# Optimization experiments

Hardware: AMD Instinct MI355X
Metric: run time of the kernel (lower is better)

Reference implementation:

```python
import jax, jax.numpy as jnp
import numpy as np

EPS = 1e-5
SEQ = 64

def ln(x, g, b):
    m = jnp.mean(x, axis=-1, keepdims=True)
    v = jnp.var(x, axis=-1, keepdims=True)
    return (x - m) / jnp.sqrt(v + EPS) * g + b

def gelu(x):
    return jax.nn.gelu(x, approximate=False)  # torch nn.GELU default = exact erf

def setup_inputs() -> dict:
    key = jax.random.key(0)
    ks = jax.random.split(key, 24)
    B, D = 512, 128
    DSGU = 4 * D          # 512
    DATTN = DSGU // 2     # 256
    DEXP = 4 * D          # 512 (tiny-attn expanded dim)
    TF = SEQ * D          # 8192
    H = int(1.1 * TF)     # 9011
    w = lambda k, s: jax.random.normal(k, s, dtype=jnp.float32) * 0.02
    return {
        "x": jax.random.normal(ks[0], (B, SEQ, D), dtype=jnp.float32),
        # TinyAttentionBlock
        "qkv_ln_g": jnp.ones((D,), jnp.float32), "qkv_ln_b": jnp.zeros((D,), jnp.float32),
        "qkv_w": w(ks[1], (D, 3 * DEXP)), "qkv_b": jnp.zeros((3 * DEXP,), jnp.float32),
        "attn_proj_w": w(ks[2], (DEXP, DATTN)), "attn_proj_b": jnp.zeros((DATTN,), jnp.float32),
        "attn_ln_g": jnp.ones((DATTN,), jnp.float32), "attn_ln_b": jnp.zeros((DATTN,), jnp.float32),
        "rel_bias": w(ks[3], (2 * SEQ - 1,)),
        "scale": jnp.asarray(1.0 / np.sqrt(D), jnp.float32),
        # SGU proj_in / proj_spatial / proj_out
        "pin_ln_g": jnp.ones((D,), jnp.float32), "pin_ln_b": jnp.zeros((D,), jnp.float32),
        "pin_w": w(ks[4], (D, DSGU)), "pin_b": jnp.zeros((DSGU,), jnp.float32),
        "sp_ln_g": jnp.ones((SEQ,), jnp.float32), "sp_ln_b": jnp.zeros((SEQ,), jnp.float32),
        "sp_w": w(ks[5], (SEQ, SEQ)), "sp_b": jnp.ones((SEQ,), jnp.float32),  # bias init 1.0 per source
        "pout_ln_g": jnp.ones((DATTN,), jnp.float32), "pout_ln_b": jnp.zeros((DATTN,), jnp.float32),
        "pout_w": w(ks[6], (DATTN, D)), "pout_b": jnp.zeros((D,), jnp.float32),
        # ResidualBlock MLP
        "mlp_ln_g": jnp.ones((TF,), jnp.float32), "mlp_ln_b": jnp.zeros((TF,), jnp.float32),
        "mlp_w1": w(ks[7], (TF, H)), "mlp_b1": jnp.zeros((H,), jnp.float32),
        "mlp_w2": w(ks[8], (H, TF)), "mlp_b2": jnp.zeros((TF,), jnp.float32),
    }

def reference(x, qkv_ln_g, qkv_ln_b, qkv_w, qkv_b, attn_proj_w, attn_proj_b,
              attn_ln_g, attn_ln_b, rel_bias, scale,
              pin_ln_g, pin_ln_b, pin_w, pin_b, sp_ln_g, sp_ln_b, sp_w, sp_b,
              pout_ln_g, pout_ln_b, pout_w, pout_b,
              mlp_ln_g, mlp_ln_b, mlp_w1, mlp_b1, mlp_w2, mlp_b2):
    B = x.shape[0]
    # --- TinyAttentionBlock ---
    h = ln(x, qkv_ln_g, qkv_ln_b) @ qkv_w + qkv_b          # [B,64,3*512]
    q, k, v = jnp.split(h, 3, axis=-1)                      # each [B,64,512]
    idx = jnp.arange(SEQ)
    rel = idx[None, :] - idx[:, None] + (SEQ - 1)           # [64,64] in [0,126]
    bias = rel_bias[rel]                                    # [64,64]
    attn = jnp.einsum('bnd,bmd->bnm', q, k) + bias
    attn = jax.nn.softmax(attn, axis=-1) * scale            # post-softmax scale (as in source)
    av = jnp.einsum('bnm,bmd->bnd', attn, v)                # [B,64,512]
    a = ln(av @ attn_proj_w + attn_proj_b, attn_ln_g, attn_ln_b)  # [B,64,256]
    # --- SpatialGatingUnit ---
    h2 = gelu(ln(x, pin_ln_g, pin_ln_b) @ pin_w + pin_b)    # [B,64,512]
    u, vv = jnp.split(h2, 2, axis=-1)                        # [B,64,256] each
    vt = jnp.swapaxes(vv, 1, 2)                              # [B,256,64]
    vt = gelu(ln(vt, sp_ln_g, sp_ln_b) @ sp_w + sp_b)        # spatial proj over seq dim
    vv = jnp.swapaxes(vt, 1, 2)                              # [B,64,256]
    out = u * (vv + a)
    out = ln(out, pout_ln_g, pout_ln_b) @ pout_w + pout_b    # [B,64,128]
    x = x + out
    # --- ResidualBlock MLP on flattened board ---
    xf = x.reshape(B, -1)                                    # [B,8192]
    h3 = gelu(ln(xf, mlp_ln_g, mlp_ln_b) @ mlp_w1 + mlp_b1)  # [B,9011]
    xf = xf + (h3 @ mlp_w2 + mlp_b2)
    return xf.reshape(B, SEQ, -1)
```

## Files before the change

kernel.cpp:

```cpp
#include <hip/hip_runtime.h>
#include <hip/hip_bf16.h>
#include <math.h>

typedef float f32x4 __attribute__((ext_vector_type(4)));
typedef float f32x2 __attribute__((ext_vector_type(2)));
typedef short s16x8 __attribute__((ext_vector_type(8)));
typedef short s16x4 __attribute__((ext_vector_type(4)));
typedef int   i32x4 __attribute__((ext_vector_type(4)));

__device__ __forceinline__ short f2bf(float f) {
  __hip_bfloat16 h = __float2bfloat16(f);
  return __builtin_bit_cast(short, h);
}
__device__ __forceinline__ float bf2f(short s) {
  __hip_bfloat16 h = __builtin_bit_cast(__hip_bfloat16, s);
  return __bfloat162float(h);
}
__device__ __forceinline__ float gelu_f(float x) {
  return 0.5f * x * (1.f + erff(x * 0.70710678118654752440f));
}
__device__ __forceinline__ float waveSum(float v) {
  #pragma unroll
  for (int d = 32; d; d >>= 1) v += __shfl_xor(v, d);
  return v;
}
__device__ __forceinline__ void softBarrier() {
  asm volatile("s_waitcnt lgkmcnt(0)" ::: "memory");
  __builtin_amdgcn_s_barrier();
  asm volatile("" ::: "memory");
}

__global__ __launch_bounds__(256) void fused_attn_k(
    const float* __restrict__ x,
    const float* __restrict__ qln_g, const float* __restrict__ qln_b,
    const float* __restrict__ pln_g, const float* __restrict__ pln_b,
    const float* __restrict__ qkv_w, const float* __restrict__ qkv_b,
    const float* __restrict__ attn_pw, const float* __restrict__ attn_pb,
    const float* __restrict__ aln_g, const float* __restrict__ aln_b,
    const float* __restrict__ relb, const float* __restrict__ scale_p,
    short* __restrict__ lnp, float* __restrict__ ab)
{
  __shared__ __align__(16) char arena[153088];
  short (*lnq)[136]  = reinterpret_cast<short(*)[136]>(arena + 0);
  short (*plds)[72]  = reinterpret_cast<short(*)[72]>(arena + 17408);
  short (*vlds)[72]  = reinterpret_cast<short(*)[72]>(arena + 26624);
  short (*avl)[136]  = reinterpret_cast<short(*)[136]>(arena + 26624);
  short (*qlds)[136] = reinterpret_cast<short(*)[136]>(arena + 45056);
  short (*klds)[136] = reinterpret_cast<short(*)[136]>(arena + 62464);
  short (*pwT)[128]  = reinterpret_cast<short(*)[128]>(arena + 45056);
  short (*wT)[128]   = reinterpret_cast<short(*)[128]>(arena + 110592);
  float* rb    = reinterpret_cast<float*>(arena + 143360);
  float* s_apb = reinterpret_cast<float*>(arena + 143872);
  float* s_ag  = reinterpret_cast<float*>(arena + 144896);
  float* s_ab2 = reinterpret_cast<float*>(arena + 145920);
  float* sqb   = reinterpret_cast<float*>(arena + 146944);

  const int t = threadIdx.x, lane = t & 63, w = t >> 6;
  const int ln15 = lane & 15, hi = lane >> 4;
  const int b = blockIdx.x;

  if (t < 127) rb[t] = relb[t];
  s_apb[t] = attn_pb[t]; s_ag[t] = aln_g[t]; s_ab2[t] = aln_b[t];
  #pragma unroll
  for (int i = 0; i < 6; ++i) sqb[i*256 + t] = qkv_b[i*256 + t];

  {
    int c = lane * 2;
    float qg0 = qln_g[c], qg1 = qln_g[c+1], qb0 = qln_b[c], qb1 = qln_b[c+1];
    float pg0 = pln_g[c], pg1 = pln_g[c+1], pb0 = pln_b[c], pb1 = pln_b[c+1];
    for (int i = 0; i < 16; ++i) {
      int r = w * 16 + i;
      f32x2 v = *reinterpret_cast<const f32x2*>(&x[((size_t)b*64 + r)*128 + c]);
      float s = v[0] + v[1], sq = v[0]*v[0] + v[1]*v[1];
      s = waveSum(s); sq = waveSum(sq);
      float m = s * (1.f/128.f);
      float rstd = rsqrtf(sq*(1.f/128.f) - m*m + 1e-5f);
      float a0 = (v[0]-m)*rstd, a1 = (v[1]-m)*rstd;
      unsigned q0 = (unsigned short)f2bf(a0*qg0 + qb0);
      unsigned q1 = (unsigned short)f2bf(a1*qg1 + qb1);
      *reinterpret_cast<unsigned*>(&lnq[r][c]) = q0 | (q1 << 16);
      unsigned p0 = (unsigned short)f2bf(a0*pg0 + pb0);
      unsigned p1 = (unsigned short)f2bf(a1*pg1 + pb1);
      ((unsigned*)lnp)[((size_t)b*64 + r)*64 + lane] = p0 | (p1 << 16);
    }
  }
  __syncthreads();

  auto stageW = [&](int coff) {
    const int c = t & 127, h = t >> 7;
    #pragma unroll
    for (int j = 0; j < 8; ++j) {
      int o = h * 8 + j;
      s16x8 v;
      #pragma unroll
      for (int m = 0; m < 8; ++m)
        v[m] = f2bf(qkv_w[(size_t)(o*8 + m) * 1536 + coff + c]);
      int os = (o & 8) | ((o & 7) ^ (c & 7));
      *reinterpret_cast<s16x8*>(&wT[c][os * 8]) = v;
    }
  };
  auto stagePW = [&](int cc) {
    const int c = t;
    #pragma unroll
    for (int o = 0; o < 16; ++o) {
      s16x8 v;
      #pragma unroll
      for (int m = 0; m < 8; ++m)
        v[m] = f2bf(attn_pw[(size_t)(cc*128 + o*8 + m) * 256 + c]);
      int os = (o & 8) | ((o & 7) ^ (c & 7));
      *reinterpret_cast<s16x8*>(&pwT[c][os * 8]) = v;
    }
  };
  auto gemm8 = [&](f32x4 (&acc)[8]) {
    #pragma unroll
    for (int kk = 0; kk < 4; ++kk) {
      s16x8 af = *reinterpret_cast<const s16x8*>(&lnq[w*16 + ln15][kk*32 + hi*8]);
      const int o = kk*4 + hi;
      #pragma unroll
      for (int fn = 0; fn < 8; ++fn) {
        int col = fn*16 + ln15;
        int os = (o & 8) | ((o & 7) ^ (col & 7));
        s16x8 bf = *reinterpret_cast<const s16x8*>(&wT[col][os * 8]);
        acc[fn] = __builtin_amdgcn_mfma_f32_16x16x32_bf16(af, bf, acc[fn], 0, 0, 0);
      }
    }
  };

  f32x4 sacc[4] = {};
  for (int kc = 0; kc < 4; ++kc) {
    __syncthreads();
    stageW(kc * 128);
    __syncthreads();
    {
      f32x4 qa[8] = {};
      gemm8(qa);
      #pragma unroll
      for (int fn = 0; fn < 8; ++fn) {
        float bias = sqb[kc*128 + fn*16 + ln15];
        #pragma unroll
        for (int j = 0; j < 4; ++j)
          qlds[w*16 + hi*4 + j][fn*16 + ln15] = f2bf(qa[fn][j] + bias);
      }
    }
    __syncthreads();
    stageW(512 + kc * 128);
    __syncthreads();
    {
      f32x4 ka[8] = {};
      gemm8(ka);
      #pragma unroll
      for (int fn = 0; fn < 8; ++fn) {
        float bias = sqb[512 + kc*128 + fn*16 + ln15];
        #pragma unroll
        for (int j = 0; j < 4; ++j)
          klds[w*16 + hi*4 + j][fn*16 + ln15] = f2bf(ka[fn][j] + bias);
      }
    }
    __syncthreads();
    #pragma unroll
    for (int kk = 0; kk < 4; ++kk) {
      s16x8 aq = *reinterpret_cast<const s16x8*>(&qlds[16*w + ln15][kk*32 + hi*8]);
      #pragma unroll
      for (int fn = 0; fn < 4; ++fn) {
        s16x8 bk = *reinterpret_cast<const s16x8*>(&klds[fn*16 + ln15][kk*32 + hi*8]);
        sacc[fn] = __builtin_amdgcn_mfma_f32_16x16x32_bf16(aq, bk, sacc[fn], 0, 0, 0);
      }
    }
  }

  {
    float scale = scale_p[0];
    #pragma unroll
    for (int j = 0; j < 4; ++j) {
      int row = 16*w + hi*4 + j;
      float pv[4];
      float mx = -1e30f;
      #pragma unroll
      for (int fn = 0; fn < 4; ++fn) {
        int col = fn*16 + ln15;
        pv[fn] = sacc[fn][j] + rb[col - row + 63];
        mx = fmaxf(mx, pv[fn]);
      }
      #pragma unroll
      for (int d = 1; d < 16; d <<= 1) mx = fmaxf(mx, __shfl_xor(mx, d));
      float sum = 0.f;
      #pragma unroll
      for (int fn = 0; fn < 4; ++fn) { pv[fn] = __expf(pv[fn] - mx); sum += pv[fn]; }
      #pragma unroll
      for (int d = 1; d < 16; d <<= 1) sum += __shfl_xor(sum, d);
      float inv = scale / sum;
      #pragma unroll
      for (int fn = 0; fn < 4; ++fn) plds[row][fn*16 + ln15] = f2bf(pv[fn] * inv);
    }
  }

  f32x4 pracc[16] = {};
  for (int cc = 0; cc < 4; ++cc) {
    __syncthreads();
    stageW(1024 + cc * 128);
    stagePW(cc);
    __syncthreads();
    {
      f32x4 va[8] = {};
      gemm8(va);
      #pragma unroll
      for (int fn = 0; fn < 8; ++fn) {
        float bias = sqb[1024 + cc*128 + fn*16 + ln15];
        s16x4 vv;
        #pragma unroll
        for (int j = 0; j < 4; ++j) vv[j] = f2bf(va[fn][j] + bias);
        *reinterpret_cast<s16x4*>(&vlds[fn*16 + ln15][w*16 + hi*4]) = vv;
      }
    }
    __syncthreads();
    f32x4 pacc[8] = {};
    #pragma unroll
    for (int kk = 0; kk < 2; ++kk) {
      s16x8 ap = *reinterpret_cast<const s16x8*>(&plds[16*w + ln15][kk*32 + hi*8]);
      #pragma unroll
      for (int fn = 0; fn < 8; ++fn) {
        s16x8 bv = *reinterpret_cast<const s16x8*>(&vlds[fn*16 + ln15][kk*32 + hi*8]);
        pacc[fn] = __builtin_amdgcn_mfma_f32_16x16x32_bf16(ap, bv, pacc[fn], 0, 0, 0);
      }
    }
    __syncthreads();
    #pragma unroll
    for (int fn = 0; fn < 8; ++fn)
      #pragma unroll
      for (int j = 0; j < 4; ++j)
        avl[w*16 + hi*4 + j][fn*16 + ln15] = f2bf(pacc[fn][j]);
    __syncthreads();
    #pragma unroll
    for (int kk = 0; kk < 4; ++kk) {
      s16x8 aa = *reinterpret_cast<const s16x8*>(&avl[16*w + ln15][kk*32 + hi*8]);
      const int o = kk*4 + hi;
      #pragma unroll
      for (int fn = 0; fn < 16; ++fn) {
        int col = fn*16 + ln15;
        int os = (o & 8) | ((o & 7) ^ (col & 7));
        s16x8 pb = *reinterpret_cast<const s16x8*>(&pwT[col][os * 8]);
        pracc[fn] = __builtin_amdgcn_mfma_f32_16x16x32_bf16(aa, pb, pracc[fn], 0, 0, 0);
      }
    }
  }

  #pragma unroll
  for (int j = 0; j < 4; ++j) {
    int row = 16*w + hi*4 + j;
    float vv[16];
    float s = 0.f, sq = 0.f;
    #pragma unroll
    for (int fn = 0; fn < 16; ++fn) {
      vv[fn] = pracc[fn][j] + s_apb[fn*16 + ln15];
      s += vv[fn]; sq += vv[fn]*vv[fn];
    }
    #pragma unroll
    for (int d = 1; d < 16; d <<= 1) { s += __shfl_xor(s, d); sq += __shfl_xor(sq, d); }
    float m = s * (1.f/256.f);
    float rstd = rsqrtf(sq*(1.f/256.f) - m*m + 1e-5f);
    #pragma unroll
    for (int fn = 0; fn < 16; ++fn) {
      int col = fn*16 + ln15;
      ab[((size_t)b*64 + row)*256 + col] = (vv[fn]-m)*rstd*s_ag[col] + s_ab2[col];
    }
  }
}

template<int BM, int BN, int WM, int WN, int EPI>
__global__ __launch_bounds__(256) void gemm_k(
    const short* __restrict__ A, const float* __restrict__ Bw,
    const float* __restrict__ bias, const float* __restrict__ res,
    void* __restrict__ O0, void* __restrict__ O1,
    int M, int N, int K, int Nreal, int Kreal)
{
  constexpr int BK = 64;
  __shared__ __align__(16) short As[BM][BK + 8];
  __shared__ __align__(16) short Bs[BN][BK + 8];
  const int t = threadIdx.x;
  const int lane = t & 63;
  const int w = t >> 6;
  const int wm = w / WN, wn = w % WN;
  const int ln15 = lane & 15, hi = lane >> 4;
  const int m0 = blockIdx.y * BM;
  const int n0 = blockIdx.x * BN;

  f32x4 acc[4][4] = {};

  for (int k0 = 0; k0 < K; k0 += BK) {
    #pragma unroll
    for (int i = 0; i < (BM*BK)/(256*8); ++i) {
      int e = (i*256 + t) * 8;
      int r = e / BK, c = e % BK;
      *reinterpret_cast<i32x4*>(&As[r][c]) =
          *reinterpret_cast<const i32x4*>(&A[(size_t)(m0 + r) * K + k0 + c]);
    }
    #pragma unroll
    for (int i = 0; i < (BK*BN)/256; ++i) {
      int idx = i*256 + t;
      int n = idx % BN, k = idx / BN;
      int gk = k0 + k, gn = n0 + n;
      float v = (gk < Kreal && gn < Nreal) ? Bw[(size_t)gk * Nreal + gn] : 0.f;
      Bs[n][k] = f2bf(v);
    }
    __syncthreads();
    #pragma unroll
    for (int kk = 0; kk < BK; kk += 32) {
      s16x8 af[4], bfr[4];
      #pragma unroll
      for (int fm = 0; fm < 4; ++fm)
        af[fm] = *reinterpret_cast<const s16x8*>(&As[wm*64 + fm*16 + ln15][kk + hi*8]);
      #pragma unroll
      for (int fn = 0; fn < 4; ++fn)
        bfr[fn] = *reinterpret_cast<const s16x8*>(&Bs[wn*64 + fn*16 + ln15][kk + hi*8]);
      #pragma unroll
      for (int fm = 0; fm < 4; ++fm)
        #pragma unroll
        for (int fn = 0; fn < 4; ++fn)
          acc[fm][fn] = __builtin_amdgcn_mfma_f32_16x16x32_bf16(
              af[fm], bfr[fn], acc[fm][fn], 0, 0, 0);
    }
    __syncthreads();
  }

  #pragma unroll
  for (int fm = 0; fm < 4; ++fm) {
    #pragma unroll
    for (int fn = 0; fn < 4; ++fn) {
      #pragma unroll
      for (int j = 0; j < 4; ++j) {
        int row = m0 + wm*64 + fm*16 + hi*4 + j;
        int col = n0 + wn*64 + fn*16 + ln15;
        float v = acc[fm][fn][j];
        if constexpr (EPI == 2) {
          v = gelu_f(v + bias[col]);
          if (col < 256) ((float*)O0)[(size_t)row * 256 + col] = v;
          else ((short*)O1)[(size_t)row * 256 + (col - 256)] = f2bf(v);
        } else {
          v += bias[col] + res[(size_t)row * N + col];
          ((float*)O0)[(size_t)row * N + col] = v;
        }
      }
    }
  }
}

__global__ __launch_bounds__(256) void ln8192_k(
    const float* __restrict__ x1,
    const float* __restrict__ g, const float* __restrict__ bb,
    short* __restrict__ lnxp)
{
  __shared__ float red[8];
  int t = threadIdx.x, w = t >> 6, lane = t & 63;
  int b = blockIdx.x;
  const f32x4* xr = reinterpret_cast<const f32x4*>(x1 + (size_t)b * 8192);
  f32x4 vals[8];
  float s = 0.f, sq = 0.f;
  #pragma unroll
  for (int i = 0; i < 8; ++i) {
    f32x4 v = xr[t + i*256];
    vals[i] = v;
    s  += v[0]+v[1]+v[2]+v[3];
    sq += v[0]*v[0]+v[1]*v[1]+v[2]*v[2]+v[3]*v[3];
  }
  s = waveSum(s); sq = waveSum(sq);
  if (lane == 0) { red[w] = s; red[4+w] = sq; }
  __syncthreads();
  s  = red[0]+red[1]+red[2]+red[3];
  sq = red[4]+red[5]+red[6]+red[7];
  float m = s * (1.f/8192.f);
  float rstd = rsqrtf(sq * (1.f/8192.f) - m*m + 1e-5f);
  #pragma unroll
  for (int i = 0; i < 8; ++i) {
    int idx = (t + i*256) * 4;
    f32x4 g4 = reinterpret_cast<const f32x4*>(g)[t + i*256];
    f32x4 b4 = reinterpret_cast<const f32x4*>(bb)[t + i*256];
    s16x4 o;
    #pragma unroll
    for (int k = 0; k < 4; ++k) o[k] = f2bf((vals[i][k]-m)*rstd*g4[k] + b4[k]);
    size_t paddr = ((size_t)(idx >> 6) * 512 + b) * 64 + (idx & 63);
    *reinterpret_cast<s16x4*>(&lnxp[paddr]) = o;
  }
}

__global__ __launch_bounds__(512, 2) void gemm_splitk9(
    const short* __restrict__ Ap, const float* __restrict__ Bw,
    float* __restrict__ part,
    int N, int K, int Kreal, int ldb, int kchunk, int ntiles)
{
  __shared__ __align__(16) short Bs[2][128 * 64];
  const int t = threadIdx.x, lane = t & 63, w = t >> 6;
  const int ln15 = lane & 15, hi = lane >> 4;
  const int nt = blockIdx.x % ntiles, z = blockIdx.x / ntiles;
  const int n0 = nt * 128;
  const int kbeg = z * kchunk;
  const int kend = (kbeg + kchunk < K) ? (kbeg + kchunk) : K;
  const int nsteps = (kend - kbeg) >> 6;

  const int bn = t & 127;
  const int bg0 = (t >> 7) * 2;
  const bool bok = (n0 + bn) < ldb;
  const int bsw = bn & 7;

  float br[16];
  auto loadB = [&](int k0) {
    const float* bp = Bw + (size_t)(k0 + bg0 * 8) * ldb + n0 + bn;
    #pragma unroll
    for (int m = 0; m < 16; ++m) {
      int gk = k0 + bg0 * 8 + m;
      br[m] = (bok && gk < Kreal) ? bp[(size_t)m * ldb] : 0.f;
    }
  };
  auto writeB = [&](int buf) {
    s16x8 v0, v1;
    #pragma unroll
    for (int m = 0; m < 8; ++m) { v0[m] = f2bf(br[m]); v1[m] = f2bf(br[8 + m]); }
    short* dst = &Bs[buf][bn * 64];
    *reinterpret_cast<s16x8*>(dst + ((bg0    ) ^ bsw) * 8) = v0;
    *reinterpret_cast<s16x8*>(dst + ((bg0 + 1) ^ bsw) * 8) = v1;
  };

  f32x4 acc[4][8] = {};

  loadB(kbeg);
  writeB(0);
  if (nsteps > 1) loadB(kbeg + 64);
  softBarrier();

  for (int s = 0; s < nsteps; ++s) {
    const int k0 = kbeg + s * 64;
    const short* atile = Ap + (size_t)(k0 >> 6) * 512 * 64;
    s16x8 af[8];
    #pragma unroll
    for (int kk = 0; kk < 2; ++kk)
      #pragma unroll
      for (int fm = 0; fm < 4; ++fm) {
        int row = w * 64 + fm * 16 + ln15;
        af[kk * 4 + fm] = *reinterpret_cast<const s16x8*>(
            &atile[row * 64 + (kk * 4 + hi) * 8]);
      }
    if (s + 1 < nsteps) writeB((s + 1) & 1);
    if (s + 2 < nsteps) loadB(kbeg + (s + 2) * 64);

    const short* bsrc = &Bs[s & 1][0];
    #pragma unroll
    for (int kk = 0; kk < 2; ++kk) {
      const int g = kk * 4 + hi;
      #pragma unroll
      for (int fn = 0; fn < 8; ++fn) {
        int row = fn * 16 + ln15;
        s16x8 bv = *reinterpret_cast<const s16x8*>(
            &bsrc[row * 64 + ((g ^ (row & 7)) * 8)]);
        #pragma unroll
        for (int fm = 0; fm < 4; ++fm)
          acc[fm][fn] = __builtin_amdgcn_mfma_f32_16x16x32_bf16(
              af[kk * 4 + fm], bv, acc[fm][fn], 0, 0, 0);
      }
    }
    softBarrier();
  }

  #pragma unroll
  for (int fm = 0; fm < 4; ++fm)
    #pragma unroll
    for (int fn = 0; fn < 8; ++fn)
      #pragma unroll
      for (int j = 0; j < 4; ++j) {
        int row = w * 64 + fm * 16 + hi * 4 + j;
        int col = n0 + fn * 16 + ln15;
        part[((size_t)z * 512 + row) * N + col] = acc[fm][fn][j];
      }
}

__global__ __launch_bounds__(256) void reduce_mlp1_k(
    const float* __restrict__ part, const float* __restrict__ bias,
    short* __restrict__ h3p, int N, int Nreal, int M, int ks)
{
  int col4 = (blockIdx.x * 256 + threadIdx.x) * 4;
  int row = blockIdx.y;
  if (col4 >= N) return;
  size_t base = (size_t)row * N + col4;
  size_t stride = (size_t)M * N;
  f32x4 s = *reinterpret_cast<const f32x4*>(part + base);
  for (int k = 1; k < ks; ++k)
    s += *reinterpret_cast<const f32x4*>(part + base + (size_t)k * stride);
  s16x4 o;
  #pragma unroll
  for (int j = 0; j < 4; ++j) {
    int c = col4 + j;
    float v = 0.f;
    if (c < Nreal) v = gelu_f(s[j] + bias[c]);
    o[j] = f2bf(v);
  }
  size_t paddr = ((size_t)(col4 >> 6) * 512 + row) * 64 + (col4 & 63);
  *reinterpret_cast<s16x4*>(&h3p[paddr]) = o;
}

__global__ __launch_bounds__(256) void reduce_mlp2_k(
    const float* __restrict__ part, const float* __restrict__ bias,
    const float* __restrict__ x1, float* __restrict__ out, int N, int M, int ks)
{
  int col4 = (blockIdx.x * 256 + threadIdx.x) * 4;
  int row = blockIdx.y;
  size_t base = (size_t)row * N + col4;
  size_t stride = (size_t)M * N;
  f32x4 s = *reinterpret_cast<const f32x4*>(part + base);
  for (int k = 1; k < ks; ++k)
    s += *reinterpret_cast<const f32x4*>(part + base + (size_t)k * stride);
  f32x4 b4 = *reinterpret_cast<const f32x4*>(bias + col4);
  f32x4 r4 = *reinterpret_cast<const f32x4*>(x1 + base);
  #pragma unroll
  for (int j = 0; j < 4; ++j) s[j] += b4[j] + r4[j];
  *reinterpret_cast<f32x4*>(out + base) = s;
}

__global__ __launch_bounds__(256) void gate_k(
    const float* __restrict__ u, const short* __restrict__ vbf,
    const float* __restrict__ a,
    const float* __restrict__ spg_g, const float* __restrict__ spg_b,
    const float* __restrict__ spw, const float* __restrict__ spb,
    const float* __restrict__ pog, const float* __restrict__ pob,
    short* __restrict__ outn)
{
  __shared__ __align__(16) short nvb[256][72];
  __shared__ __align__(16) short spwT[64][72];
  __shared__ float s_spg[64], s_spbl[64], s_spb[64];
  __shared__ float s_pog[256], s_pob[256];
  int t = threadIdx.x, lane = t & 63, w = t >> 6;
  int ln15 = lane & 15, hi = lane >> 4;
  int b = blockIdx.x;

  if (t < 64) { s_spg[t] = spg_g[t]; s_spbl[t] = spg_b[t]; s_spb[t] = spb[t]; }
  s_pog[t] = pog[t]; s_pob[t] = pob[t];
  #pragma unroll
  for (int i = 0; i < 16; ++i) {
    int idx = i*256 + t;
    int sr = idx >> 6, tc = idx & 63;
    spwT[tc][sr] = f2bf(spw[idx]);
  }

  float vvv[64];
  {
    int c = t;
    float s = 0.f, sq = 0.f;
    #pragma unroll
    for (int si = 0; si < 64; ++si) {
      float f = bf2f(vbf[(size_t)(b*64 + si) * 256 + c]);
      vvv[si] = f; s += f; sq += f*f;
    }
    float m = s * (1.f/64.f);
    float rstd = rsqrtf(sq * (1.f/64.f) - m*m + 1e-5f);
    __syncthreads();
    #pragma unroll
    for (int si = 0; si < 64; ++si)
      nvb[c][si] = f2bf((vvv[si]-m)*rstd*s_spg[si] + s_spbl[si]);
  }
  __syncthreads();

  f32x4 yacc[4][4] = {};
  #pragma unroll
  for (int kk = 0; kk < 64; kk += 32) {
    s16x8 af[4], bfr[4];
    #pragma unroll
    for (int fm = 0; fm < 4; ++fm)
      af[fm] = *reinterpret_cast<const s16x8*>(&nvb[64*w + fm*16 + ln15][kk + hi*8]);
    #pragma unroll
    for (int fn = 0; fn < 4; ++fn)
      bfr[fn] = *reinterpret_cast<const s16x8*>(&spwT[fn*16 + ln15][kk + hi*8]);
    #pragma unroll
    for (int fm = 0; fm < 4; ++fm)
      #pragma unroll
      for (int fn = 0; fn < 4; ++fn)
        yacc[fm][fn] = __builtin_amdgcn_mfma_f32_16x16x32_bf16(
            af[fm], bfr[fn], yacc[fm][fn], 0, 0, 0);
  }
  __syncthreads();

  short (*outl)[264] = reinterpret_cast<short(*)[264]>(&nvb[0][0]);
  #pragma unroll
  for (int fm = 0; fm < 4; ++fm) {
    #pragma unroll
    for (int fn = 0; fn < 4; ++fn) {
      int crow = 64*w + fm*16 + hi*4;
      int tcol = fn*16 + ln15;
      f32x4 u4 = *reinterpret_cast<const f32x4*>(&u[(size_t)(b*64 + tcol)*256 + crow]);
      f32x4 a4 = *reinterpret_cast<const f32x4*>(&a[(size_t)(b*64 + tcol)*256 + crow]);
      #pragma unroll
      for (int j = 0; j < 4; ++j) {
        float g = gelu_f(yacc[fm][fn][j] + s_spb[tcol]);
        float o = u4[j] * (g + a4[j]);
        outl[tcol][crow + j] = f2bf(o);
      }
    }
  }
  __syncthreads();

  #pragma unroll
  for (int ri = 0; ri < 16; ++ri) {
    int trow = w*16 + ri;
    int c = lane * 4;
    s16x4 raw = *reinterpret_cast<const s16x4*>(&outl[trow][c]);
    float f0 = bf2f(raw[0]), f1 = bf2f(raw[1]), f2 = bf2f(raw[2]), f3 = bf2f(raw[3]);
    float s  = f0+f1+f2+f3;
    float sq = f0*f0+f1*f1+f2*f2+f3*f3;
    s = waveSum(s); sq = waveSum(sq);
    float m = s * (1.f/256.f);
    float rstd = rsqrtf(sq * (1.f/256.f) - m*m + 1e-5f);
    s16x4 o;
    o[0] = f2bf((f0-m)*rstd*s_pog[c+0] + s_pob[c+0]);
    o[1] = f2bf((f1-m)*rstd*s_pog[c+1] + s_pob[c+1]);
    o[2] = f2bf((f2-m)*rstd*s_pog[c+2] + s_pob[c+2]);
    o[3] = f2bf((f3-m)*rstd*s_pog[c+3] + s_pob[c+3]);
    *reinterpret_cast<s16x4*>(&outn[(size_t)(b*64 + trow)*256 + c]) = o;
  }
}

extern "C" void kernel_launch(void* const* d_in, const int* in_sizes, int n_in,
                              void* d_out, int out_size, void* d_ws, size_t ws_size,
                              hipStream_t stream)
{
  const float* x          = (const float*)d_in[0];
  const float* qkv_ln_g   = (const float*)d_in[1];
  const float* qkv_ln_b   = (const float*)d_in[2];
  const float* qkv_w      = (const float*)d_in[3];
  const float* qkv_b      = (const float*)d_in[4];
  const float* attn_pw    = (const float*)d_in[5];
  const float* attn_pb    = (const float*)d_in[6];
  const float* attn_ln_g  = (const float*)d_in[7];
  const float* attn_ln_b  = (const float*)d_in[8];
  const float* rel_bias   = (const float*)d_in[9];
  const float* scale      = (const float*)d_in[10];
  const float* pin_ln_g   = (const float*)d_in[11];
  const float* pin_ln_b   = (const float*)d_in[12];
  const float* pin_w      = (const float*)d_in[13];
  const float* pin_b      = (const float*)d_in[14];
  const float* sp_ln_g    = (const float*)d_in[15];
  const float* sp_ln_b    = (const float*)d_in[16];
  const float* sp_w       = (const float*)d_in[17];
  const float* sp_b       = (const float*)d_in[18];
  const float* pout_ln_g  = (const float*)d_in[19];
  const float* pout_ln_b  = (const float*)d_in[20];
  const float* pout_w     = (const float*)d_in[21];
  const float* pout_b     = (const float*)d_in[22];
  const float* mlp_ln_g   = (const float*)d_in[23];
  const float* mlp_ln_b   = (const float*)d_in[24];
  const float* mlp_w1     = (const float*)d_in[25];
  const float* mlp_b1     = (const float*)d_in[26];
  const float* mlp_w2     = (const float*)d_in[27];
  const float* mlp_b2     = (const float*)d_in[28];

  char* ws = (char*)d_ws;
  short* lnp   = (short*)(ws + 0);
  float* x1b   = (float*)(ws + 0);
  float* ab    = (float*)(ws + 16777216);
  float* ub    = (float*)(ws + 50331648);
  short* vbfb  = (short*)(ws + 83886080);
  short* outnb = (short*)(ws + 100663296);
  short* lnxp  = (short*)(ws + 150994944);
  short* h3p   = (short*)(ws + 159383552);
  float* partb = (float*)(ws + 16777216);

  fused_attn_k<<<512, 256, 0, stream>>>(
      x, qkv_ln_g, qkv_ln_b, pin_ln_g, pin_ln_b, qkv_w, qkv_b,
      attn_pw, attn_pb, attn_ln_g, attn_ln_b, rel_bias, scale, lnp, ab);
  gemm_k<128,128,2,2,2><<<dim3(4,256), 256, 0, stream>>>(
      lnp, pin_w, pin_b, nullptr, ub, vbfb, 32768, 512, 128, 512, 128);
  gate_k<<<512, 256, 0, stream>>>(ub, vbfb, ab, sp_ln_g, sp_ln_b, sp_w, sp_b,
                                  pout_ln_g, pout_ln_b, outnb);
  gemm_k<128,128,2,2,3><<<dim3(1,256), 256, 0, stream>>>(
      outnb, pout_w, pout_b, x, x1b, nullptr, 32768, 128, 256, 128, 256);
  ln8192_k<<<512, 256, 0, stream>>>(x1b, mlp_ln_g, mlp_ln_b, lnxp);

  gemm_splitk9<<<213, 512, 0, stream>>>(
      lnxp, mlp_w1, partb, 9088, 8192, 8192,
      9011, 2752, 71);
  reduce_mlp1_k<<<dim3(9, 512), 256, 0, stream>>>(partb, mlp_b1, h3p, 9088, 9011, 512, 3);

  gemm_splitk9<<<256, 512, 0, stream>>>(
      h3p, mlp_w2, partb, 8192, 9088, 9011,
      8192, 2304, 64);
  reduce_mlp2_k<<<dim3(8, 512), 256, 0, stream>>>(partb, mlp_b2, x1b, (float*)d_out, 8192, 512, 4);
}
```

Baseline: 718.6 us.

## Pre-transpose attention weights to bf16 once and read them from global in fused attention

Adds a small prep kernel that converts the qkv and attention-projection weights to transposed bf16 once per call. The fused attention kernel then reads MFMA B-operands directly from global/L2 instead of staging and converting the weights into LDS in every block. This shrinks LDS from about 150KB to about 73KB so two blocks can share a CU, and it reworks the QK loop into 64-wide chunks. The cost is one extra launch and operand loads that are uncoalesced global reads rather than LDS reads.

```diff
diff --git a/kernel.cpp b/kernel.cpp
--- a/kernel.cpp
+++ b/kernel.cpp
@@ -30,37 +30,58 @@
   asm volatile("" ::: "memory");
 }
 
-__global__ __launch_bounds__(256) void fused_attn_k(
+__global__ __launch_bounds__(256) void prep_w_k(
+    const float* __restrict__ qkv_w, const float* __restrict__ attn_pw,
+    short* __restrict__ wTg, short* __restrict__ pwTg)
+{
+  int idx = blockIdx.x * 256 + threadIdx.x;
+  if (idx < 24576) {
+    int r = idx >> 4;
+    int k0 = (idx & 15) * 8;
+    s16x8 v;
+    #pragma unroll
+    for (int m = 0; m < 8; ++m) v[m] = f2bf(qkv_w[(size_t)(k0 + m) * 1536 + r]);
+    *reinterpret_cast<s16x8*>(&wTg[r * 128 + k0]) = v;
+  } else if (idx < 24576 + 16384) {
+    int e = idx - 24576;
+    int r = e >> 6;
+    int k0 = (e & 63) * 8;
+    s16x8 v;
+    #pragma unroll
+    for (int m = 0; m < 8; ++m) v[m] = f2bf(attn_pw[(size_t)(k0 + m) * 256 + r]);
+    *reinterpret_cast<s16x8*>(&pwTg[r * 512 + k0]) = v;
+  }
+}
+
+__global__ __launch_bounds__(256, 2) void fused_attn_k(
     const float* __restrict__ x,
     const float* __restrict__ qln_g, const float* __restrict__ qln_b,
     const float* __restrict__ pln_g, const float* __restrict__ pln_b,
-    const float* __restrict__ qkv_w, const float* __restrict__ qkv_b,
-    const float* __restrict__ attn_pw, const float* __restrict__ attn_pb,
+    const short* __restrict__ wTg, const float* __restrict__ qkv_b,
+    const short* __restrict__ pwTg, const float* __restrict__ attn_pb,
     const float* __restrict__ aln_g, const float* __restrict__ aln_b,
     const float* __restrict__ relb, const float* __restrict__ scale_p,
     short* __restrict__ lnp, float* __restrict__ ab)
 {
-  __shared__ __align__(16) char arena[153088];
-  short (*lnq)[136]  = reinterpret_cast<short(*)[136]>(arena + 0);
-  short (*plds)[72]  = reinterpret_cast<short(*)[72]>(arena + 17408);
-  short (*vlds)[72]  = reinterpret_cast<short(*)[72]>(arena + 26624);
-  short (*avl)[136]  = reinterpret_cast<short(*)[136]>(arena + 26624);
-  short (*qlds)[136] = reinterpret_cast<short(*)[136]>(arena + 45056);
-  short (*klds)[136] = reinterpret_cast<short(*)[136]>(arena + 62464);
-  short (*pwT)[128]  = reinterpret_cast<short(*)[128]>(arena + 45056);
-  short (*wT)[128]   = reinterpret_cast<short(*)[128]>(arena + 110592);
-  float* rb    = reinterpret_cast<float*>(arena + 143360);
-  float* s_apb = reinterpret_cast<float*>(arena + 143872);
-  float* s_ag  = reinterpret_cast<float*>(arena + 144896);
-  float* s_ab2 = reinterpret_cast<float*>(arena + 145920);
-  float* sqb   = reinterpret_cast<float*>(arena + 146944);
+  __shared__ __align__(16) char arena[73216];
+  short (*lnq)[136] = reinterpret_cast<short(*)[136]>(arena + 0);
+  short (*vlds)[72] = reinterpret_cast<short(*)[72]>(arena + 17408);
+  short (*avl)[136] = reinterpret_cast<short(*)[136]>(arena + 17408);
+  short (*q64)[72]  = reinterpret_cast<short(*)[72]>(arena + 35840);
+  short (*k64)[72]  = reinterpret_cast<short(*)[72]>(arena + 45056);
+  short (*p64)[72]  = reinterpret_cast<short(*)[72]>(arena + 54272);
+  float* sqb  = reinterpret_cast<float*>(arena + 63488);
+  float* rb   = reinterpret_cast<float*>(arena + 69632);
+  float* sapb = reinterpret_cast<float*>(arena + 70144);
+  float* sag  = reinterpret_cast<float*>(arena + 71168);
+  float* sab2 = reinterpret_cast<float*>(arena + 72192);
 
   const int t = threadIdx.x, lane = t & 63, w = t >> 6;
   const int ln15 = lane & 15, hi = lane >> 4;
   const int b = blockIdx.x;
 
   if (t < 127) rb[t] = relb[t];
-  s_apb[t] = attn_pb[t]; s_ag[t] = aln_g[t]; s_ab2[t] = aln_b[t];
+  sapb[t] = attn_pb[t]; sag[t] = aln_g[t]; sab2[t] = aln_b[t];
   #pragma unroll
   for (int i = 0; i < 6; ++i) sqb[i*256 + t] = qkv_b[i*256 + t];
 
@@ -76,9 +97,9 @@
       float m = s * (1.f/128.f);
       float rstd = rsqrtf(sq*(1.f/128.f) - m*m + 1e-5f);
       float a0 = (v[0]-m)*rstd, a1 = (v[1]-m)*rstd;
-      unsigned q0 = (unsigned short)f2bf(a0*qg0 + qb0);
-      unsigned q1 = (unsigned short)f2bf(a1*qg1 + qb1);
-      *reinterpret_cast<unsigned*>(&lnq[r][c]) = q0 | (q1 << 16);
+      unsigned u0 = (unsigned short)f2bf(a0*qg0 + qb0);
+      unsigned u1 = (unsigned short)f2bf(a1*qg1 + qb1);
+      *reinterpret_cast<unsigned*>(&lnq[r][c]) = u0 | (u1 << 16);
       unsigned p0 = (unsigned short)f2bf(a0*pg0 + pb0);
       unsigned p1 = (unsigned short)f2bf(a1*pg1 + pb1);
       ((unsigned*)lnp)[((size_t)b*64 + r)*64 + lane] = p0 | (p1 << 16);
@@ -86,83 +107,59 @@
   }
   __syncthreads();
 
-  auto stageW = [&](int coff) {
-    const int c = t & 127, h = t >> 7;
-    #pragma unroll
-    for (int j = 0; j < 8; ++j) {
-      int o = h * 8 + j;
-      s16x8 v;
-      #pragma unroll
-      for (int m = 0; m < 8; ++m)
-        v[m] = f2bf(qkv_w[(size_t)(o*8 + m) * 1536 + coff + c]);
-      int os = (o & 8) | ((o & 7) ^ (c & 7));
-      *reinterpret_cast<s16x8*>(&wT[c][os * 8]) = v;
-    }
-  };
-  auto stagePW = [&](int cc) {
-    const int c = t;
-    #pragma unroll
-    for (int o = 0; o < 16; ++o) {
-      s16x8 v;
-      #pragma unroll
-      for (int m = 0; m < 8; ++m)
-        v[m] = f2bf(attn_pw[(size_t)(cc*128 + o*8 + m) * 256 + c]);
-      int os = (o & 8) | ((o & 7) ^ (c & 7));
-      *reinterpret_cast<s16x8*>(&pwT[c][os * 8]) = v;
-    }
-  };
-  auto gemm8 = [&](f32x4 (&acc)[8]) {
+  auto gemm4g = [&](int coff, f32x4 (&acc)[4]) {
     #pragma unroll
     for (int kk = 0; kk < 4; ++kk) {
       s16x8 af = *reinterpret_cast<const s16x8*>(&lnq[w*16 + ln15][kk*32 + hi*8]);
-      const int o = kk*4 + hi;
+      #pragma unroll
+      for (int fn = 0; fn < 4; ++fn) {
+        int col = coff + fn*16 + ln15;
+        s16x8 bf = *reinterpret_cast<const s16x8*>(&wTg[(size_t)col*128 + kk*32 + hi*8]);
+        acc[fn] = __builtin_amdgcn_mfma_f32_16x16x32_bf16(af, bf, acc[fn], 0, 0, 0);
+      }
+    }
+  };
+  auto gemm8g = [&](int coff, f32x4 (&acc)[8]) {
+    #pragma unroll
+    for (int kk = 0; kk < 4; ++kk) {
+      s16x8 af = *reinterpret_cast<const s16x8*>(&lnq[w*16 + ln15][kk*32 + hi*8]);
       #pragma unroll
       for (int fn = 0; fn < 8; ++fn) {
-        int col = fn*16 + ln15;
-        int os = (o & 8) | ((o & 7) ^ (col & 7));
-        s16x8 bf = *reinterpret_cast<const s16x8*>(&wT[col][os * 8]);
+        int col = coff + fn*16 + ln15;
+        s16x8 bf = *reinterpret_cast<const s16x8*>(&wTg[(size_t)col*128 + kk*32 + hi*8]);
         acc[fn] = __builtin_amdgcn_mfma_f32_16x16x32_bf16(af, bf, acc[fn], 0, 0, 0);
       }
     }
   };
 
   f32x4 sacc[4] = {};
-  for (int kc = 0; kc < 4; ++kc) {
-    __syncthreads();
-    stageW(kc * 128);
-    __syncthreads();
-    {
-      f32x4 qa[8] = {};
-      gemm8(qa);
-      #pragma unroll
-      for (int fn = 0; fn < 8; ++fn) {
-        float bias = sqb[kc*128 + fn*16 + ln15];
-        #pragma unroll
-        for (int j = 0; j < 4; ++j)
-          qlds[w*16 + hi*4 + j][fn*16 + ln15] = f2bf(qa[fn][j] + bias);
-      }
-    }
-    __syncthreads();
-    stageW(512 + kc * 128);
-    __syncthreads();
-    {
-      f32x4 ka[8] = {};
-      gemm8(ka);
-      #pragma unroll
-      for (int fn = 0; fn < 8; ++fn) {
-        float bias = sqb[512 + kc*128 + fn*16 + ln15];
-        #pragma unroll
-        for (int j = 0; j < 4; ++j)
-          klds[w*16 + hi*4 + j][fn*16 + ln15] = f2bf(ka[fn][j] + bias);
-      }
-    }
-    __syncthreads();
-    #pragma unroll
-    for (int kk = 0; kk < 4; ++kk) {
-      s16x8 aq = *reinterpret_cast<const s16x8*>(&qlds[16*w + ln15][kk*32 + hi*8]);
+  for (int kc = 0; kc < 8; ++kc) {
+    __syncthreads();
+    f32x4 qa[4] = {};
+    gemm4g(kc * 64, qa);
+    #pragma unroll
+    for (int fn = 0; fn < 4; ++fn) {
+      float bias = sqb[kc*64 + fn*16 + ln15];
+      #pragma unroll
+      for (int j = 0; j < 4; ++j)
+        q64[w*16 + hi*4 + j][fn*16 + ln15] = f2bf(qa[fn][j] + bias);
+    }
+    f32x4 ka[4] = {};
+    gemm4g(512 + kc * 64, ka);
+    #pragma unroll
+    for (int fn = 0; fn < 4; ++fn) {
+      float bias = sqb[512 + kc*64 + fn*16 + ln15];
+      #pragma unroll
+      for (int j = 0; j < 4; ++j)
+        k64[w*16 + hi*4 + j][fn*16 + ln15] = f2bf(ka[fn][j] + bias);
+    }
+    __syncthreads();
+    #pragma unroll
+    for (int kk = 0; kk < 2; ++kk) {
+      s16x8 aq = *reinterpret_cast<const s16x8*>(&q64[16*w + ln15][kk*32 + hi*8]);
       #pragma unroll
       for (int fn = 0; fn < 4; ++fn) {
-        s16x8 bk = *reinterpret_cast<const s16x8*>(&klds[fn*16 + ln15][kk*32 + hi*8]);
+        s16x8 bk = *reinterpret_cast<const s16x8*>(&k64[fn*16 + ln15][kk*32 + hi*8]);
         sacc[fn] = __builtin_amdgcn_mfma_f32_16x16x32_bf16(aq, bk, sacc[fn], 0, 0, 0);
       }
     }
@@ -190,33 +187,28 @@
       for (int d = 1; d < 16; d <<= 1) sum += __shfl_xor(sum, d);
       float inv = scale / sum;
       #pragma unroll
-      for (int fn = 0; fn < 4; ++fn) plds[row][fn*16 + ln15] = f2bf(pv[fn] * inv);
+      for (int fn = 0; fn < 4; ++fn) p64[row][fn*16 + ln15] = f2bf(pv[fn] * inv);
     }
   }
 
   f32x4 pracc[16] = {};
   for (int cc = 0; cc < 4; ++cc) {
     __syncthreads();
-    stageW(1024 + cc * 128);
-    stagePW(cc);
-    __syncthreads();
-    {
-      f32x4 va[8] = {};
-      gemm8(va);
-      #pragma unroll
-      for (int fn = 0; fn < 8; ++fn) {
-        float bias = sqb[1024 + cc*128 + fn*16 + ln15];
-        s16x4 vv;
-        #pragma unroll
-        for (int j = 0; j < 4; ++j) vv[j] = f2bf(va[fn][j] + bias);
-        *reinterpret_cast<s16x4*>(&vlds[fn*16 + ln15][w*16 + hi*4]) = vv;
-      }
+    f32x4 va[8] = {};
+    gemm8g(1024 + cc * 128, va);
+    #pragma unroll
+    for (int fn = 0; fn < 8; ++fn) {
+      float bias = sqb[1024 + cc*128 + fn*16 + ln15];
+      s16x4 vv;
+      #pragma unroll
+      for (int j = 0; j < 4; ++j) vv[j] = f2bf(va[fn][j] + bias);
+      *reinterpret_cast<s16x4*>(&vlds[fn*16 + ln15][w*16 + hi*4]) = vv;
     }
     __syncthreads();
     f32x4 pacc[8] = {};
     #pragma unroll
     for (int kk = 0; kk < 2; ++kk) {
-      s16x8 ap = *reinterpret_cast<const s16x8*>(&plds[16*w + ln15][kk*32 + hi*8]);
+      s16x8 ap = *reinterpret_cast<const s16x8*>(&p64[16*w + ln15][kk*32 + hi*8]);
       #pragma unroll
       for (int fn = 0; fn < 8; ++fn) {
         s16x8 bv = *reinterpret_cast<const s16x8*>(&vlds[fn*16 + ln15][kk*32 + hi*8]);
@@ -233,12 +225,10 @@
     #pragma unroll
     for (int kk = 0; kk < 4; ++kk) {
       s16x8 aa = *reinterpret_cast<const s16x8*>(&avl[16*w + ln15][kk*32 + hi*8]);
-      const int o = kk*4 + hi;
       #pragma unroll
       for (int fn = 0; fn < 16; ++fn) {
-        int col = fn*16 + ln15;
-        int os = (o & 8) | ((o & 7) ^ (col & 7));
-        s16x8 pb = *reinterpret_cast<const s16x8*>(&pwT[col][os * 8]);
+        s16x8 pb = *reinterpret_cast<const s16x8*>(
+            &pwTg[(size_t)(fn*16 + ln15)*512 + cc*128 + kk*32 + hi*8]);
         pracc[fn] = __builtin_amdgcn_mfma_f32_16x16x32_bf16(aa, pb, pracc[fn], 0, 0, 0);
       }
     }
@@ -251,7 +241,7 @@
     float s = 0.f, sq = 0.f;
     #pragma unroll
     for (int fn = 0; fn < 16; ++fn) {
-      vv[fn] = pracc[fn][j] + s_apb[fn*16 + ln15];
+      vv[fn] = pracc[fn][j] + sapb[fn*16 + ln15];
       s += vv[fn]; sq += vv[fn]*vv[fn];
     }
     #pragma unroll
@@ -261,7 +251,7 @@
     #pragma unroll
     for (int fn = 0; fn < 16; ++fn) {
       int col = fn*16 + ln15;
-      ab[((size_t)b*64 + row)*256 + col] = (vv[fn]-m)*rstd*s_ag[col] + s_ab2[col];
+      ab[((size_t)b*64 + row)*256 + col] = (vv[fn]-m)*rstd*sag[col] + sab2[col];
     }
   }
 }
@@ -653,15 +643,18 @@
   float* x1b   = (float*)(ws + 0);
   float* ab    = (float*)(ws + 16777216);
   float* ub    = (float*)(ws + 50331648);
+  short* wTg   = (short*)(ws + 83886080);
+  short* pwTg  = (short*)(ws + 84279296);
   short* vbfb  = (short*)(ws + 83886080);
   short* outnb = (short*)(ws + 100663296);
   short* lnxp  = (short*)(ws + 150994944);
   short* h3p   = (short*)(ws + 159383552);
   float* partb = (float*)(ws + 16777216);
 
+  prep_w_k<<<160, 256, 0, stream>>>(qkv_w, attn_pw, wTg, pwTg);
   fused_attn_k<<<512, 256, 0, stream>>>(
-      x, qkv_ln_g, qkv_ln_b, pin_ln_g, pin_ln_b, qkv_w, qkv_b,
-      attn_pw, attn_pb, attn_ln_g, attn_ln_b, rel_bias, scale, lnp, ab);
+      x, qkv_ln_g, qkv_ln_b, pin_ln_g, pin_ln_b, wTg, qkv_b,
+      pwTg, attn_pb, attn_ln_g, attn_ln_b, rel_bias, scale, lnp, ab);
   gemm_k<128,128,2,2,2><<<dim3(4,256), 256, 0, stream>>>(
       lnp, pin_w, pin_b, nullptr, ub, vbfb, 32768, 512, 128, 512, 128);
   gate_k<<<512, 256, 0, stream>>>(ub, vbfb, ab, sp_ln_g, sp_ln_b, sp_w, sp_b,
```

New measurement: 649.1 us, median of 2. 9.7% less time.
